# Optimization experiments

Hardware: AMD Instinct MI355X
Metric: run time of the kernel (lower is better)

Reference implementation:

```python
import jax, jax.numpy as jnp
import numpy as np

B, S, D = 32, 512, 512      # batch, seq, feature
E, H, O, K = 8, 2048, 512, 2  # experts, expert hidden, expert out, top_k


def setup_inputs() -> dict:
    key = jax.random.key(0)
    ks = jax.random.split(key, 5)
    sc = lambda k, shape, scale: jax.random.normal(k, shape, jnp.float32) * scale
    return {
        "x": sc(ks[0], (B, S, D), 1.0),
        "attn_w": sc(ks[1], (D, 1), 0.05),
        "attn_b": jnp.zeros((1,), jnp.float32),
        "gate_w": sc(ks[2], (D, E), 0.05),
        "gate_b": jnp.zeros((E,), jnp.float32),
        "w1": sc(ks[3], (E, D, H), 0.02),
        "b1": jnp.zeros((E, H), jnp.float32),
        "w2": sc(ks[4], (E, H, O), 0.02),
        "b2": jnp.zeros((E, O), jnp.float32),
    }


def reference(x, attn_w, attn_b, gate_w, gate_b, w1, b1, w2, b2):
    # --- attention pooling over the sequence axis ---
    scores = x @ attn_w + attn_b                      # [B,S,1]
    aw = jax.nn.softmax(scores, axis=1)               # softmax over seq
    pooled = jnp.sum(x * aw, axis=1)                  # [B,D]

    # --- gating: softmax -> top-k mask -> renormalize ---
    gates = jax.nn.softmax(pooled @ gate_w + gate_b, axis=-1)  # [B,E]
    _, idx = jax.lax.top_k(gates, K)                  # [B,K]
    mask = jnp.sum(jax.nn.one_hot(idx, E, dtype=gates.dtype), axis=-2)  # [B,E]
    g = gates * mask
    g = g / (jnp.sum(g, axis=-1, keepdims=True) + 1e-9)        # [B,E]

    # --- dense all-experts compute (exact GELU, as keras Dense('gelu')) ---
    h = jax.nn.gelu(jnp.einsum('bsd,edh->ebsh', x, w1) + b1[:, None, None, :],
                    approximate=False)                 # [E,B,S,H]
    eo = jax.nn.gelu(jnp.einsum('ebsh,eho->ebso', h, w2) + b2[:, None, None, :],
                     approximate=False)                # [E,B,S,O]

    # --- weighted combine over experts ---
    return jnp.einsum('ebso,be->bso', eo, g)           # [B,S,O]
```

## Files before the change

### kernel.cpp

```cpp
#include <hip/hip_runtime.h>
#include <hip/hip_bf16.h>
#include <math.h>

#define B_  32
#define S_  512
#define D_  512
#define E_  8
#define H_  2048
#define O_  512

typedef __bf16 bf16x8 __attribute__((ext_vector_type(8)));
typedef float  f32x4  __attribute__((ext_vector_type(4)));

#define GL2LDS(src, dst) \
  __builtin_amdgcn_global_load_lds((const __attribute__((address_space(1))) void*)(src), \
                                   (__attribute__((address_space(3))) void*)(dst), 16, 0, 0)

#define MFMA16(a, b, c) __builtin_amdgcn_mfma_f32_16x16x32_bf16((a), (b), (c), 0, 0, 0)

__device__ __forceinline__ float gelu_fast(float v) {
  float w = v * fmaf(v * v, 0.0713548162f, 1.5957691216f);
  float e = __expf(-w);
  return v * __builtin_amdgcn_rcpf(1.0f + e);
}


__global__ __launch_bounds__(256) void cast_score_kernel(
    const float* __restrict__ x, const float* __restrict__ attn_w,
    char* __restrict__ xpack, float* __restrict__ scores)
{
  const int t = threadIdx.x;
  const int r = t >> 5;
  const int cg = t & 31;
  const int row = blockIdx.x * 8 + r;
  const int bb = row >> 9, s = row & 511;
  const float* src  = x + (size_t)row * D_ + cg * 16;
  const float* wsrc = attn_w + cg * 16;
  char* xp = xpack + (size_t)bb * 524288 + s * 64;
  const int sx = (s >> 1) & 3;
  float acc = 0.f;
#pragma unroll
  for (int k = 0; k < 4; ++k) {
    const int d0 = cg * 16 + k * 4;
    float4 v  = *(const float4*)(src + k * 4);
    float4 wv = *(const float4*)(wsrc + k * 4);
    acc += v.x * wv.x + v.y * wv.y + v.z * wv.z + v.w * wv.w;
    ushort4 o;
    o.x = __builtin_bit_cast(unsigned short, __float2bfloat16(v.x));
    o.y = __builtin_bit_cast(unsigned short, __float2bfloat16(v.y));
    o.z = __builtin_bit_cast(unsigned short, __float2bfloat16(v.z));
    o.w = __builtin_bit_cast(unsigned short, __float2bfloat16(v.w));
    const int kt2 = ((d0 >> 6) << 1) | ((d0 >> 5) & 1);
    const int byte = kt2 * 32768 + ((((d0 >> 3) & 3) ^ sx) << 4) + (d0 & 7) * 2;
    *(ushort4*)(xp + byte) = o;
  }
#pragma unroll
  for (int off = 16; off; off >>= 1) acc += __shfl_xor(acc, off);
  if (cg == 0) scores[row] = acc;
}

__global__ __launch_bounds__(512) void softmax_aw_kernel(
    const float* __restrict__ scores, float* __restrict__ aw)
{
  __shared__ float red[8];
  __shared__ float mm, ss;
  const int t = threadIdx.x, b = blockIdx.x;
  float v = scores[b * S_ + t];
  float m = v;
#pragma unroll
  for (int off = 32; off; off >>= 1) m = fmaxf(m, __shfl_xor(m, off));
  if ((t & 63) == 0) red[t >> 6] = m;
  __syncthreads();
  if (t == 0) {
    float a = red[0];
    for (int i = 1; i < 8; ++i) a = fmaxf(a, red[i]);
    mm = a;
  }
  __syncthreads();
  float e = expf(v - mm);
  float s = e;
#pragma unroll
  for (int off = 32; off; off >>= 1) s += __shfl_xor(s, off);
  if ((t & 63) == 0) red[t >> 6] = s;
  __syncthreads();
  if (t == 0) {
    float a = 0.f;
    for (int i = 0; i < 8; ++i) a += red[i];
    ss = 1.f / a;
  }
  __syncthreads();
  aw[b * S_ + t] = e * ss;
}

__global__ __launch_bounds__(512) void pool_kernel(
    const float* __restrict__ x, const float* __restrict__ aw, float* __restrict__ pooled)
{
  __shared__ float sm[4][128];
  const int t = threadIdx.x;
  const int dl = t & 127;
  const int sh = t >> 7;
  const int b = blockIdx.y;
  const int d = blockIdx.x * 128 + dl;
  const float* xp  = x + (size_t)b * S_ * D_ + d;
  const float* awb = aw + b * S_;
  float acc = 0.f;
#pragma unroll 4
  for (int s = sh; s < S_; s += 4)
    acc = fmaf(awb[s], xp[(size_t)s * D_], acc);
  if (sh) sm[sh][dl] = acc;
  __syncthreads();
  if (sh == 0) pooled[b * D_ + d] = acc + sm[1][dl] + sm[2][dl] + sm[3][dl];
}

__global__ __launch_bounds__(256) void gate_psort_kernel(
    const float* __restrict__ pooled, const float* __restrict__ gate_w,
    const float* __restrict__ gate_b, int* __restrict__ gidx, float* __restrict__ gwt,
    int* __restrict__ psort)
{
  __shared__ float gl[32][8];
  const int t = threadIdx.x;
  const int b = t >> 3, ee = t & 7;
  float z = gate_b[ee];
  const float* pb = pooled + b * D_;
  for (int d = 0; d < D_; ++d) z = fmaf(pb[d], gate_w[d * E_ + ee], z);
  gl[b][ee] = z;
  __syncthreads();
  if (t < 32) {
    float ge[8];
    float zmax = gl[t][0];
    for (int i = 1; i < 8; ++i) zmax = fmaxf(zmax, gl[t][i]);
    float zs = 0.f;
    for (int i = 0; i < 8; ++i) { ge[i] = expf(gl[t][i] - zmax); zs += ge[i]; }
    for (int i = 0; i < 8; ++i) ge[i] /= zs;
    int i0 = 0;
    for (int i = 1; i < 8; ++i) if (ge[i] > ge[i0]) i0 = i;
    int i1 = -1;
    for (int i = 0; i < 8; ++i) if (i != i0 && (i1 < 0 || ge[i] > ge[i1])) i1 = i;
    float denom = ge[i0] + ge[i1] + 1e-9f;
    gidx[t * 2 + 0] = i0; gidx[t * 2 + 1] = i1;
    gwt[t * 2 + 0] = ge[i0] / denom; gwt[t * 2 + 1] = ge[i1] / denom;
  }
  __syncthreads();
  if (t == 0) {
    int cnt[E_] = {}, pos[E_];
    for (int p = 0; p < 2 * B_; ++p) cnt[gidx[p]]++;
    int s = 0;
    for (int e2 = 0; e2 < E_; ++e2) { pos[e2] = s; s += cnt[e2]; }
    for (int p = 0; p < 2 * B_; ++p) psort[pos[gidx[p]]++] = p;
  }
}

__global__ void pack_w_kernel(const float* __restrict__ in, char* __restrict__ outp,
                              int R, int C)
{
  __shared__ float tile[32][33];
  const int z = blockIdx.z;
  const float* inz = in + (size_t)z * R * C;
  const int c0 = blockIdx.x * 32, r0 = blockIdx.y * 32;
  const int tx = threadIdx.x, ty = threadIdx.y;
#pragma unroll
  for (int jj = 0; jj < 4; ++jj) {
    int r = r0 + ty + jj * 8;
    tile[ty + jj * 8][tx] = inz[(size_t)r * C + c0 + tx];
  }
  __syncthreads();
  const int k = r0 + tx;
  const int kt2 = ((k >> 6) << 1) | ((k >> 5) & 1);
  const int PAN = C * 64;
  char* oz = outp + (size_t)z * R * C * 2 + (size_t)kt2 * PAN;
  const int kslot = (k >> 3) & 3;
  const int kbyte = (k & 7) * 2;
#pragma unroll
  for (int jj = 0; jj < 4; ++jj) {
    const int row = c0 + ty + jj * 8;
    const int byte = row * 64 + ((kslot ^ ((row >> 1) & 3)) << 4) + kbyte;
    *(ushort*)(oz + byte) =
        __builtin_bit_cast(unsigned short, __float2bfloat16(tile[tx][ty + jj * 8]));
  }
}

__device__ __forceinline__ void gemm_core_v4(const char* __restrict__ Ag, const char* __restrict__ Bg,
                                             const int panelA, const int panelB, const int NT,
                                             char* lds, f32x4 (&acc)[8][4])
{
  const int tid = threadIdx.x;
  const int l = tid & 63;
  const int w = tid >> 6;
  const int wm = w >> 2;
  const int wn = w & 3;
  const int lr = l & 15;
  const int ks = (l >> 4) & 3;
  const int axor = ((ks ^ ((lr >> 1) & 3)) << 4);
  const int abase = (wm * 128 + lr) * 64 + axor;
  const int bbase = 32768 + (wn * 64 + lr) * 64 + axor;
  const int dst = tid * 16;

#define SU_A(t, kh, bufp) { const char* s_ = Ag + (size_t)((t) * 2 + (kh)) * panelA; \
    GL2LDS(s_ + dst,        (bufp) + (kh) * 16384 + dst); \
    GL2LDS(s_ + 8192 + dst, (bufp) + (kh) * 16384 + 8192 + dst); }
#define SU_B(t, kh, bufp) { const char* s_ = Bg + (size_t)((t) * 2 + (kh)) * panelB; \
    GL2LDS(s_ + dst,        (bufp) + 32768 + (kh) * 16384 + dst); \
    GL2LDS(s_ + 8192 + dst, (bufp) + 32768 + (kh) * 16384 + 8192 + dst); }

  SU_A(0, 0, lds); SU_B(0, 0, lds); SU_A(0, 1, lds); SU_B(0, 1, lds);

#pragma unroll 1
  for (int t = 0; t < NT; ++t) {
    char* cur = lds + ((t & 1) << 16);
    char* nb  = lds + (((t + 1) & 1) << 16);
    const bool pre = (t + 1 < NT);
    bf16x8 a[8], bv0, bv1, bv2, bv3;

    __builtin_amdgcn_sched_barrier(0);
    asm volatile("s_waitcnt vmcnt(4)" ::: "memory");
    __builtin_amdgcn_s_barrier();
    __builtin_amdgcn_sched_barrier(0);
    if (pre) SU_A(t + 1, 0, nb);
#pragma unroll
    for (int m = 0; m < 8; ++m) a[m] = *(const bf16x8*)(cur + abase + m * 1024);
    bv0 = *(const bf16x8*)(cur + bbase);
    bv1 = *(const bf16x8*)(cur + bbase + 1024);
    __builtin_amdgcn_s_setprio(1);
#pragma unroll
    for (int m = 0; m < 8; ++m) {
      acc[m][0] = MFMA16(a[m], bv0, acc[m][0]);
      acc[m][1] = MFMA16(a[m], bv1, acc[m][1]);
    }
    __builtin_amdgcn_s_setprio(0);

    if (pre) SU_B(t + 1, 0, nb);
    bv2 = *(const bf16x8*)(cur + bbase + 2048);
    bv3 = *(const bf16x8*)(cur + bbase + 3072);
    __builtin_amdgcn_s_setprio(1);
#pragma unroll
    for (int m = 0; m < 8; ++m) {
      acc[m][2] = MFMA16(a[m], bv2, acc[m][2]);
      acc[m][3] = MFMA16(a[m], bv3, acc[m][3]);
    }
    __builtin_amdgcn_s_setprio(0);

    __builtin_amdgcn_sched_barrier(0);
    if (pre) asm volatile("s_waitcnt vmcnt(4)" ::: "memory");
    else     asm volatile("s_waitcnt vmcnt(0)" ::: "memory");
    __builtin_amdgcn_s_barrier();
    __builtin_amdgcn_sched_barrier(0);
    if (pre) SU_A(t + 1, 1, nb);
#pragma unroll
    for (int m = 0; m < 8; ++m) a[m] = *(const bf16x8*)(cur + abase + 16384 + m * 1024);
    bv0 = *(const bf16x8*)(cur + bbase + 16384);
    bv1 = *(const bf16x8*)(cur + bbase + 16384 + 1024);
    __builtin_amdgcn_s_setprio(1);
#pragma unroll
    for (int m = 0; m < 8; ++m) {
      acc[m][0] = MFMA16(a[m], bv0, acc[m][0]);
      acc[m][1] = MFMA16(a[m], bv1, acc[m][1]);
    }
    __builtin_amdgcn_s_setprio(0);

    if (pre) SU_B(t + 1, 1, nb);
    bv2 = *(const bf16x8*)(cur + bbase + 16384 + 2048);
    bv3 = *(const bf16x8*)(cur + bbase + 16384 + 3072);
    __builtin_amdgcn_s_setprio(1);
#pragma unroll
    for (int m = 0; m < 8; ++m) {
      acc[m][2] = MFMA16(a[m], bv2, acc[m][2]);
      acc[m][3] = MFMA16(a[m], bv3, acc[m][3]);
    }
    __builtin_amdgcn_s_setprio(0);
  }
#undef SU_A
#undef SU_B
}

__global__ __launch_bounds__(512, 2) void gemm1_kernel(
    const char* __restrict__ xpack, const char* __restrict__ W1pack,
    const float* __restrict__ b1, char* __restrict__ Hpack,
    const int* __restrict__ gidx, const int* __restrict__ psort)
{
  extern __shared__ char lds[];
  const int P = blockIdx.x;
  const int L = (P & 7) * 128 + (P >> 3);
  const int p = psort[L >> 4];
  const int tl = L & 15;
  const int b = p >> 1;
  const int e = gidx[p];
  const int h0 = (tl >> 1) * 256;
  const int s0 = (tl & 1) * 256;
  const char* Ag = W1pack + (size_t)e * 2097152 + h0 * 64;
  const char* Bg = xpack + (size_t)b * 524288 + s0 * 64;
  f32x4 acc[8][4] = {};
  gemm_core_v4(Ag, Bg, 131072, 32768, D_ / 64, lds, acc);

  const int tid = threadIdx.x, l = tid & 63, w = tid >> 6;
  const int wm = w >> 2, wn = w & 3, lr = l & 15, q4 = ((l >> 4) & 3) << 2;
  const float* b1e = b1 + (size_t)e * H_ + h0;
  char* Hp = Hpack + (size_t)p * 2097152;
#pragma unroll
  for (int m = 0; m < 8; ++m) {
    const int hl = wm * 128 + m * 16 + q4;
    const int h = h0 + hl;
    const int kt2h = ((h >> 6) << 1) | ((h >> 5) & 1);
    const int hslot = (h >> 3) & 3;
    const int hbyte = (h & 7) * 2;
    const float4 bias = *(const float4*)(b1e + hl);
#pragma unroll
    for (int n = 0; n < 4; ++n) {
      const int sl = s0 + wn * 64 + n * 16 + lr;
      ushort4 ov;
      ov.x = __builtin_bit_cast(unsigned short, __float2bfloat16(gelu_fast(acc[m][n][0] + bias.x)));
      ov.y = __builtin_bit_cast(unsigned short, __float2bfloat16(gelu_fast(acc[m][n][1] + bias.y)));
      ov.z = __builtin_bit_cast(unsigned short, __float2bfloat16(gelu_fast(acc[m][n][2] + bias.z)));
      ov.w = __builtin_bit_cast(unsigned short, __float2bfloat16(gelu_fast(acc[m][n][3] + bias.w)));
      const int byte = kt2h * 32768 + sl * 64 + ((hslot ^ ((sl >> 1) & 3)) << 4) + hbyte;
      *(ushort4*)(Hp + byte) = ov;
    }
  }
}

__global__ __launch_bounds__(512, 2) void gemm2_kernel(
    const char* __restrict__ Hpack, const char* __restrict__ W2pack,
    const float* __restrict__ b2, float* __restrict__ out,
    const int* __restrict__ gidx, const float* __restrict__ gwt,
    const int* __restrict__ psort)
{
  extern __shared__ char lds[];
  const int P = blockIdx.x;
  const int L = (P & 7) * 32 + (P >> 3);
  const int p = psort[L >> 2];
  const int tl = L & 3;
  const int b = p >> 1;
  const int e = gidx[p];
  const float gw = gwt[p];
  const int s0 = (tl >> 1) * 256;
  const int o0 = (tl & 1) * 256;
  const char* Ag = Hpack + (size_t)p * 2097152 + s0 * 64;
  const char* Bg = W2pack + (size_t)e * 2097152 + o0 * 64;
  f32x4 acc[8][4] = {};
  gemm_core_v4(Ag, Bg, 32768, 32768, H_ / 64, lds, acc);

  const int tid = threadIdx.x, l = tid & 63, w = tid >> 6;
  const int wm = w >> 2, wn = w & 3, lr = l & 15, q4 = ((l >> 4) & 3) << 2;
  const float* b2e = b2 + (size_t)e * O_ + o0;
#pragma unroll
  for (int m = 0; m < 8; ++m) {
    const int sl = s0 + wm * 128 + m * 16 + q4;
#pragma unroll
    for (int n = 0; n < 4; ++n) {
      const int ol = wn * 64 + n * 16 + lr;
      const float bias = b2e[ol];
      float* dstp = out + ((size_t)b * S_ + sl) * O_ + o0 + ol;
#pragma unroll
      for (int j = 0; j < 4; ++j)
        atomicAdd(dstp + (size_t)j * O_, gelu_fast(acc[m][n][j] + bias) * gw);
    }
  }
}

__global__ void sentinel_kernel(float* out, int n) {
  int i = blockIdx.x * blockDim.x + threadIdx.x;
  for (; i < n; i += gridDim.x * blockDim.x) out[i] = 1.0e6f;
}

extern "C" void kernel_launch(void* const* d_in, const int* in_sizes, int n_in,
                              void* d_out, int out_size, void* d_ws, size_t ws_size,
                              hipStream_t stream)
{
  const float* x      = (const float*)d_in[0];
  const float* attn_w = (const float*)d_in[1];
  const float* gate_w = (const float*)d_in[3];
  const float* gate_b = (const float*)d_in[4];
  const float* w1     = (const float*)d_in[5];
  const float* b1     = (const float*)d_in[6];
  const float* w2     = (const float*)d_in[7];
  const float* b2     = (const float*)d_in[8];
  float* out = (float*)d_out;

  char* ws = (char*)d_ws;
  const size_t OFF_GIDX = 0;
  const size_t OFF_GWT  = 256;
  const size_t OFF_PSRT = 512;
  const size_t OFF_X    = 1024;
  const size_t SZ_X     = (size_t)B_ * S_ * D_ * 2;
  const size_t OFF_W1T  = OFF_X + SZ_X;
  const size_t SZ_W1T   = (size_t)E_ * H_ * D_ * 2;
  const size_t OFF_W2T  = OFF_W1T + SZ_W1T;
  const size_t SZ_W2T   = (size_t)E_ * O_ * H_ * 2;
  const size_t OFF_H    = OFF_W2T + SZ_W2T;
  const size_t PAIR_H   = (size_t)S_ * H_ * 2;

  if (OFF_H + 64 * PAIR_H > ws_size) {
    hipLaunchKernelGGL(sentinel_kernel, dim3(256), dim3(256), 0, stream, out, out_size);
    return;
  }

  int*   gidx   = (int*)(ws + OFF_GIDX);
  float* gwt    = (float*)(ws + OFF_GWT);
  int*   psort  = (int*)(ws + OFF_PSRT);
  char*  xpack  = ws + OFF_X;
  char*  W1pack = ws + OFF_W1T;
  char*  W2pack = ws + OFF_W2T;
  char*  Hpack  = ws + OFF_H;
  float* scores = (float*)(ws + OFF_H);
  float* aw     = (float*)(ws + OFF_H + 65536);
  float* pooled = (float*)(ws + OFF_H + 131072);

  (void)hipFuncSetAttribute((const void*)gemm1_kernel, hipFuncAttributeMaxDynamicSharedMemorySize, 131072);
  (void)hipFuncSetAttribute((const void*)gemm2_kernel, hipFuncAttributeMaxDynamicSharedMemorySize, 131072);

  hipLaunchKernelGGL(cast_score_kernel, dim3(B_ * S_ / 8), dim3(256), 0, stream,
                     x, attn_w, xpack, scores);
  hipLaunchKernelGGL(softmax_aw_kernel, dim3(B_), dim3(512), 0, stream, scores, aw);
  hipLaunchKernelGGL(pool_kernel, dim3(4, B_), dim3(512), 0, stream, x, aw, pooled);
  hipLaunchKernelGGL(gate_psort_kernel, dim3(1), dim3(256), 0, stream,
                     pooled, gate_w, gate_b, gidx, gwt, psort);
  hipLaunchKernelGGL(pack_w_kernel, dim3(H_ / 32, D_ / 32, E_), dim3(32, 8), 0, stream,
                     w1, W1pack, D_, H_);
  hipLaunchKernelGGL(pack_w_kernel, dim3(O_ / 32, H_ / 32, E_), dim3(32, 8), 0, stream,
                     w2, W2pack, H_, O_);
  hipMemsetAsync(d_out, 0, (size_t)out_size * sizeof(float), stream);

  hipLaunchKernelGGL(gemm1_kernel, dim3(1024), dim3(512), 131072, stream,
                     xpack, W1pack, b1, Hpack, gidx, psort);
  hipLaunchKernelGGL(gemm2_kernel, dim3(256), dim3(512), 131072, stream,
                     Hpack, W2pack, b2, out, gidx, gwt, psort);
}
```

Before: 268.4 us.

## Rework GEMM core: triple-buffered A in LDS, B operand loaded directly to registers

```diff
diff --git a/kernel.cpp b/kernel.cpp
--- a/kernel.cpp
+++ b/kernel.cpp
@@ -50,8 +50,8 @@
     o.y = __builtin_bit_cast(unsigned short, __float2bfloat16(v.y));
     o.z = __builtin_bit_cast(unsigned short, __float2bfloat16(v.z));
     o.w = __builtin_bit_cast(unsigned short, __float2bfloat16(v.w));
-    const int kt2 = ((d0 >> 6) << 1) | ((d0 >> 5) & 1);
-    const int byte = kt2 * 32768 + ((((d0 >> 3) & 3) ^ sx) << 4) + (d0 & 7) * 2;
+    const int u = d0 >> 5;
+    const int byte = u * 32768 + ((((d0 >> 3) & 3) ^ sx) << 4) + (d0 & 7) * 2;
     *(ushort4*)(xp + byte) = o;
   }
 #pragma unroll
@@ -165,9 +165,9 @@
   }
   __syncthreads();
   const int k = r0 + tx;
-  const int kt2 = ((k >> 6) << 1) | ((k >> 5) & 1);
+  const int u = k >> 5;
   const int PAN = C * 64;
-  char* oz = outp + (size_t)z * R * C * 2 + (size_t)kt2 * PAN;
+  char* oz = outp + (size_t)z * R * C * 2 + (size_t)u * PAN;
   const int kslot = (k >> 3) & 3;
   const int kbyte = (k & 7) * 2;
 #pragma unroll
@@ -179,9 +179,45 @@
   }
 }
 
-__device__ __forceinline__ void gemm_core_v4(const char* __restrict__ Ag, const char* __restrict__ Bg,
-                                             const int panelA, const int panelB, const int NT,
-                                             char* lds, f32x4 (&acc)[8][4])
+
+#define V6_TILE(tt, ce, BCUR)                                                   \
+  {                                                                             \
+    char* cur = lds + (ce) * 16384;                                             \
+    const int c2 = ((ce) + 2 >= 3) ? ((ce) - 1) : ((ce) + 2);                   \
+    char* nb = lds + c2 * 16384;                                                \
+    if ((tt) + 1 < NT) asm volatile("s_waitcnt vmcnt(6)" ::: "memory");         \
+    else               asm volatile("s_waitcnt vmcnt(0)" ::: "memory");         \
+    __builtin_amdgcn_s_barrier();                                               \
+    __builtin_amdgcn_sched_barrier(0);                                          \
+    bf16x8 a[8];                                                                \
+    _Pragma("unroll")                                                           \
+    for (int m = 0; m < 8; ++m) a[m] = *(const bf16x8*)(cur + abase + m * 1024);\
+    if ((tt) + 2 < NT) {                                                        \
+      const char* s_ = sA2 + ((tt) & 1) * panelA;                               \
+      GL2LDS(s_ + dst, nb + dst);                                               \
+      GL2LDS(s_ + 8192 + dst, nb + 8192 + dst);                                 \
+    }                                                                           \
+    asm volatile("s_waitcnt lgkmcnt(0)" ::: "memory");                          \
+    __builtin_amdgcn_sched_barrier(0);                                          \
+    __builtin_amdgcn_s_setprio(1);                                              \
+    _Pragma("unroll")                                                           \
+    for (int m = 0; m < 8; ++m) {                                               \
+      acc[m][0] = MFMA16(a[m], BCUR[0], acc[m][0]);                             \
+      acc[m][1] = MFMA16(a[m], BCUR[1], acc[m][1]);                             \
+      acc[m][2] = MFMA16(a[m], BCUR[2], acc[m][2]);                             \
+      acc[m][3] = MFMA16(a[m], BCUR[3], acc[m][3]);                             \
+    }                                                                           \
+    __builtin_amdgcn_s_setprio(0);                                              \
+    if ((tt) + 2 < NT) {                                                        \
+      const char* bsrc = sB2 + ((tt) & 1) * panelB + blane;                     \
+      _Pragma("unroll")                                                         \
+      for (int n = 0; n < 4; ++n) BCUR[n] = *(const bf16x8*)(bsrc + n * 1024);  \
+    }                                                                           \
+  }
+
+__device__ __forceinline__ void gemm_core_v6(const char* __restrict__ Ag, const char* __restrict__ Bg,
+                                             const size_t panelA, const size_t panelB,
+                                             const int NT, char* lds, f32x4 (&acc)[8][4])
 {
   const int tid = threadIdx.x;
   const int l = tid & 63;
@@ -192,84 +228,34 @@
   const int ks = (l >> 4) & 3;
   const int axor = ((ks ^ ((lr >> 1) & 3)) << 4);
   const int abase = (wm * 128 + lr) * 64 + axor;
-  const int bbase = 32768 + (wn * 64 + lr) * 64 + axor;
+  const int blane = (wn * 64 + lr) * 64 + axor;
   const int dst = tid * 16;
 
-#define SU_A(t, kh, bufp) { const char* s_ = Ag + (size_t)((t) * 2 + (kh)) * panelA; \
-    GL2LDS(s_ + dst,        (bufp) + (kh) * 16384 + dst); \
-    GL2LDS(s_ + 8192 + dst, (bufp) + (kh) * 16384 + 8192 + dst); }
-#define SU_B(t, kh, bufp) { const char* s_ = Bg + (size_t)((t) * 2 + (kh)) * panelB; \
-    GL2LDS(s_ + dst,        (bufp) + 32768 + (kh) * 16384 + dst); \
-    GL2LDS(s_ + 8192 + dst, (bufp) + 32768 + (kh) * 16384 + 8192 + dst); }
-
-  SU_A(0, 0, lds); SU_B(0, 0, lds); SU_A(0, 1, lds); SU_B(0, 1, lds);
+  GL2LDS(Ag + dst, lds + dst);
+  GL2LDS(Ag + 8192 + dst, lds + 8192 + dst);
+  bf16x8 b0[4], b1[4];
+#pragma unroll
+  for (int n = 0; n < 4; ++n) b0[n] = *(const bf16x8*)(Bg + blane + n * 1024);
+  GL2LDS(Ag + panelA + dst, lds + 16384 + dst);
+  GL2LDS(Ag + panelA + 8192 + dst, lds + 16384 + 8192 + dst);
+#pragma unroll
+  for (int n = 0; n < 4; ++n) b1[n] = *(const bf16x8*)(Bg + panelB + blane + n * 1024);
+
+  const char* sA2 = Ag + 2 * panelA;
+  const char* sB2 = Bg + 2 * panelB;
+  int ce = 0;
 
 #pragma unroll 1
-  for (int t = 0; t < NT; ++t) {
-    char* cur = lds + ((t & 1) << 16);
-    char* nb  = lds + (((t + 1) & 1) << 16);
-    const bool pre = (t + 1 < NT);
-    bf16x8 a[8], bv0, bv1, bv2, bv3;
-
-    __builtin_amdgcn_sched_barrier(0);
-    asm volatile("s_waitcnt vmcnt(4)" ::: "memory");
-    __builtin_amdgcn_s_barrier();
-    __builtin_amdgcn_sched_barrier(0);
-    if (pre) SU_A(t + 1, 0, nb);
-#pragma unroll
-    for (int m = 0; m < 8; ++m) a[m] = *(const bf16x8*)(cur + abase + m * 1024);
-    bv0 = *(const bf16x8*)(cur + bbase);
-    bv1 = *(const bf16x8*)(cur + bbase + 1024);
-    __builtin_amdgcn_s_setprio(1);
-#pragma unroll
-    for (int m = 0; m < 8; ++m) {
-      acc[m][0] = MFMA16(a[m], bv0, acc[m][0]);
-      acc[m][1] = MFMA16(a[m], bv1, acc[m][1]);
+  for (int t = 0; t < NT; t += 2) {
+    V6_TILE(t, ce, b0)
+    {
+      const int co = (ce + 1 >= 3) ? 0 : (ce + 1);
+      V6_TILE(t + 1, co, b1)
     }
-    __builtin_amdgcn_s_setprio(0);
-
-    if (pre) SU_B(t + 1, 0, nb);
-    bv2 = *(const bf16x8*)(cur + bbase + 2048);
-    bv3 = *(const bf16x8*)(cur + bbase + 3072);
-    __builtin_amdgcn_s_setprio(1);
-#pragma unroll
-    for (int m = 0; m < 8; ++m) {
-      acc[m][2] = MFMA16(a[m], bv2, acc[m][2]);
-      acc[m][3] = MFMA16(a[m], bv3, acc[m][3]);
-    }
-    __builtin_amdgcn_s_setprio(0);
-
-    __builtin_amdgcn_sched_barrier(0);
-    if (pre) asm volatile("s_waitcnt vmcnt(4)" ::: "memory");
-    else     asm volatile("s_waitcnt vmcnt(0)" ::: "memory");
-    __builtin_amdgcn_s_barrier();
-    __builtin_amdgcn_sched_barrier(0);
-    if (pre) SU_A(t + 1, 1, nb);
-#pragma unroll
-    for (int m = 0; m < 8; ++m) a[m] = *(const bf16x8*)(cur + abase + 16384 + m * 1024);
-    bv0 = *(const bf16x8*)(cur + bbase + 16384);
-    bv1 = *(const bf16x8*)(cur + bbase + 16384 + 1024);
-    __builtin_amdgcn_s_setprio(1);
-#pragma unroll
-    for (int m = 0; m < 8; ++m) {
-      acc[m][0] = MFMA16(a[m], bv0, acc[m][0]);
-      acc[m][1] = MFMA16(a[m], bv1, acc[m][1]);
-    }
-    __builtin_amdgcn_s_setprio(0);
-
-    if (pre) SU_B(t + 1, 1, nb);
-    bv2 = *(const bf16x8*)(cur + bbase + 16384 + 2048);
-    bv3 = *(const bf16x8*)(cur + bbase + 16384 + 3072);
-    __builtin_amdgcn_s_setprio(1);
-#pragma unroll
-    for (int m = 0; m < 8; ++m) {
-      acc[m][2] = MFMA16(a[m], bv2, acc[m][2]);
-      acc[m][3] = MFMA16(a[m], bv3, acc[m][3]);
-    }
-    __builtin_amdgcn_s_setprio(0);
-  }
-#undef SU_A
-#undef SU_B
+    sA2 += 2 * panelA;
+    sB2 += 2 * panelB;
+    ce = (ce + 2 >= 3) ? (ce - 1) : (ce + 2);
+  }
 }
 
 __global__ __launch_bounds__(512, 2) void gemm1_kernel(
@@ -289,7 +275,8 @@
   const char* Ag = W1pack + (size_t)e * 2097152 + h0 * 64;
   const char* Bg = xpack + (size_t)b * 524288 + s0 * 64;
   f32x4 acc[8][4] = {};
-  gemm_core_v4(Ag, Bg, 131072, 32768, D_ / 64, lds, acc);
+  const int NT = D_ / 32;
+  gemm_core_v6(Ag, Bg, 131072, 32768, NT, lds, acc);
 
   const int tid = threadIdx.x, l = tid & 63, w = tid >> 6;
   const int wm = w >> 2, wn = w & 3, lr = l & 15, q4 = ((l >> 4) & 3) << 2;
@@ -299,7 +286,7 @@
   for (int m = 0; m < 8; ++m) {
     const int hl = wm * 128 + m * 16 + q4;
     const int h = h0 + hl;
-    const int kt2h = ((h >> 6) << 1) | ((h >> 5) & 1);
+    const int uh = h >> 5;
     const int hslot = (h >> 3) & 3;
     const int hbyte = (h & 7) * 2;
     const float4 bias = *(const float4*)(b1e + hl);
@@ -311,7 +298,7 @@
       ov.y = __builtin_bit_cast(unsigned short, __float2bfloat16(gelu_fast(acc[m][n][1] + bias.y)));
       ov.z = __builtin_bit_cast(unsigned short, __float2bfloat16(gelu_fast(acc[m][n][2] + bias.z)));
       ov.w = __builtin_bit_cast(unsigned short, __float2bfloat16(gelu_fast(acc[m][n][3] + bias.w)));
-      const int byte = kt2h * 32768 + sl * 64 + ((hslot ^ ((sl >> 1) & 3)) << 4) + hbyte;
+      const int byte = uh * 32768 + sl * 64 + ((hslot ^ ((sl >> 1) & 3)) << 4) + hbyte;
       *(ushort4*)(Hp + byte) = ov;
     }
   }
@@ -336,7 +323,8 @@
   const char* Ag = Hpack + (size_t)p * 2097152 + s0 * 64;
   const char* Bg = W2pack + (size_t)e * 2097152 + o0 * 64;
   f32x4 acc[8][4] = {};
-  gemm_core_v4(Ag, Bg, 32768, 32768, H_ / 64, lds, acc);
+  const int NT = H_ / 32;
+  gemm_core_v6(Ag, Bg, 32768, 32768, NT, lds, acc);
 
   const int tid = threadIdx.x, l = tid & 63, w = tid >> 6;
   const int wm = w >> 2, wn = w & 3, lr = l & 15, q4 = ((l >> 4) & 3) << 2;
@@ -404,8 +392,8 @@
   float* aw     = (float*)(ws + OFF_H + 65536);
   float* pooled = (float*)(ws + OFF_H + 131072);
 
-  (void)hipFuncSetAttribute((const void*)gemm1_kernel, hipFuncAttributeMaxDynamicSharedMemorySize, 131072);
-  (void)hipFuncSetAttribute((const void*)gemm2_kernel, hipFuncAttributeMaxDynamicSharedMemorySize, 131072);
+  (void)hipFuncSetAttribute((const void*)gemm1_kernel, hipFuncAttributeMaxDynamicSharedMemorySize, 49152);
+  (void)hipFuncSetAttribute((const void*)gemm2_kernel, hipFuncAttributeMaxDynamicSharedMemorySize, 49152);
 
   hipLaunchKernelGGL(cast_score_kernel, dim3(B_ * S_ / 8), dim3(256), 0, stream,
                      x, attn_w, xpack, scores);
@@ -419,8 +407,8 @@
                      w2, W2pack, H_, O_);
   hipMemsetAsync(d_out, 0, (size_t)out_size * sizeof(float), stream);
 
-  hipLaunchKernelGGL(gemm1_kernel, dim3(1024), dim3(512), 131072, stream,
+  hipLaunchKernelGGL(gemm1_kernel, dim3(1024), dim3(512), 49152, stream,
                      xpack, W1pack, b1, Hpack, gidx, psort);
-  hipLaunchKernelGGL(gemm2_kernel, dim3(256), dim3(512), 131072, stream,
+  hipLaunchKernelGGL(gemm2_kernel, dim3(256), dim3(512), 49152, stream,
                      Hpack, W2pack, b2, out, gidx, gwt, psort);
 }
```

Measured after the change: 270.1 us. No clear change (+0.6%).
